# Performance work log

Hardware: AMD Instinct MI355X
Metric: run time of the kernel (lower is better)

## Reference

```python
import jax, jax.numpy as jnp
import numpy as np

N = 50000      # nodes
E = 800000     # edges (avg degree 16)
D = 64         # node_feature_dim
ED = 1         # edge_feature_dim
H = 128        # hidden_dim
G = 128        # graphs in batch
L = 3          # n_conv
EPS = 1e-5     # batchnorm eps


def setup_inputs() -> dict:
    key = jax.random.key(0)
    ks = jax.random.split(key, 20)
    w = lambda k, shp: (jax.random.normal(k, shp, dtype=jnp.float32)
                        / np.float32(np.sqrt(shp[-2] if len(shp) > 1 else 1.0)))
    return {
        "atom_z": jax.random.randint(ks[0], (N,), 0, 100),
        "edge_index": jax.random.randint(ks[1], (2, E), 0, N),
        "edge_attr": jax.random.normal(ks[2], (E, ED), dtype=jnp.float32),
        "batch": jnp.sort(jax.random.randint(ks[3], (N,), 0, G)),
        "emb": jax.random.normal(ks[4], (100, D), dtype=jnp.float32),
        "edge_W1": w(ks[5], (L, 2 * D + ED, H)), "edge_b1": jnp.zeros((L, H)),
        "edge_W2": w(ks[6], (L, H, H)),          "edge_b2": jnp.zeros((L, H)),
        "node_W1": w(ks[7], (L, D + H, H)),      "node_b1": jnp.zeros((L, H)),
        "node_W2": w(ks[8], (L, H, D)),          "node_b2": jnp.zeros((L, D)),
        "bn_gamma": jnp.ones((L, D)),            "bn_beta": jnp.zeros((L, D)),
        "out_W1": w(ks[9], (D, H)),  "out_b1": jnp.zeros((H,)),
        "out_W2": w(ks[10], (H, 1)), "out_b2": jnp.zeros((1,)),
    }


def reference(atom_z, edge_index, edge_attr, batch, emb,
              edge_W1, edge_b1, edge_W2, edge_b2,
              node_W1, node_b1, node_W2, node_b2,
              bn_gamma, bn_beta, out_W1, out_b1, out_W2, out_b2):
    sp = jax.nn.softplus
    src, dst = edge_index[0], edge_index[1]  # PyG source_to_target: x_j = x[src], x_i = x[dst]
    x = emb[atom_z]                          # [N, D]
    for l in range(L):
        # --- CGConv layer l ---
        z = jnp.concatenate([x[dst], x[src], edge_attr], axis=-1)        # [E, 2D+ED]
        m = sp(sp(z @ edge_W1[l] + edge_b1[l]) @ edge_W2[l] + edge_b2[l])  # [E, H]
        aggr = jax.ops.segment_sum(m, dst, num_segments=N)               # [N, H]
        h = jnp.concatenate([x, aggr], axis=-1)                          # [N, D+H]
        x = sp(h @ node_W1[l] + node_b1[l]) @ node_W2[l] + node_b2[l] + x
        # --- BatchNorm1d (training-mode batch stats) ---
        mu = jnp.mean(x, axis=0)
        var = jnp.mean(jnp.square(x - mu), axis=0)
        x = bn_gamma[l] * (x - mu) * jax.lax.rsqrt(var + EPS) + bn_beta[l]
    # --- global mean pool over graphs ---
    sums = jax.ops.segment_sum(x, batch, num_segments=G)                 # [G, D]
    cnts = jax.ops.segment_sum(jnp.ones((N, 1), x.dtype), batch, num_segments=G)
    pooled = sums / jnp.maximum(cnts, 1.0)
    # --- output MLP (dropout is identity at eval) ---
    out = sp(pooled @ out_W1 + out_b1) @ out_W2 + out_b2                 # [G, 1]
    return out
```

## Files before the change

kernel.cpp:

```cpp
#include <hip/hip_runtime.h>
#include <hip/hip_bf16.h>

#define N_NODES 50000
#define N_EDGES 800000
#define DIM 64
#define HID 128
#define NGRAPH 128
#define BN_EPS 1e-5f

typedef __attribute__((ext_vector_type(8))) short short8;
typedef __attribute__((ext_vector_type(4))) short short4v;
typedef __attribute__((ext_vector_type(4))) float f32x4;
typedef __attribute__((ext_vector_type(4))) int int4v;

__device__ __forceinline__ float sp_(float v) {
    return fmaxf(v, 0.f) + __logf(1.f + __expf(-fabsf(v)));
}
__device__ __forceinline__ short bfb(float f) {
    __hip_bfloat16 h = __float2bfloat16(f);
    return __builtin_bit_cast(short, h);
}
__device__ __forceinline__ float b2f(short s) {
    unsigned u = ((unsigned)(unsigned short)s) << 16;
    return __builtin_bit_cast(float, u);
}

__global__ void k_embed(const int* __restrict__ az, const float* __restrict__ emb,
                        float* __restrict__ x, __hip_bfloat16* __restrict__ xb) {
    int idx = blockIdx.x * 256 + threadIdx.x;
    if (idx >= N_NODES * DIM) return;
    int n = idx >> 6;
    int d = idx & 63;
    float v = emb[az[n] * DIM + d];
    x[idx] = v;
    xb[idx] = __float2bfloat16(v);
}

__global__ void k_wprep(const float* __restrict__ src, short* __restrict__ dst,
                        int total, int nshift, int srcStride) {
    int l = blockIdx.y;
    int idx = blockIdx.x * 256 + threadIdx.x;
    if (idx >= total) return;
    int K = total >> nshift;
    int k = idx >> nshift;
    int n = idx & ((1 << nshift) - 1);
    dst[(size_t)l * total + n * K + k] = bfb(src[(size_t)l * srcStride + idx]);
}

__global__ void k_hist(const int* __restrict__ edst, int* __restrict__ deg) {
    int e = blockIdx.x * 256 + threadIdx.x;
    if (e < N_EDGES) atomicAdd(&deg[edst[e]], 1);
}

__global__ void k_scan(const int* __restrict__ deg, int* __restrict__ cursor) {
    __shared__ int wsum[16];
    __shared__ int carry;
    const int t = threadIdx.x, lane = t & 63, w = t >> 6;
    if (t == 0) carry = 0;
    __syncthreads();
    for (int base = 0; base < N_NODES; base += 1024) {
        int i = base + t;
        int v = (i < N_NODES) ? deg[i] : 0;
        int s = v;
#pragma unroll
        for (int off = 1; off < 64; off <<= 1) {
            int u = __shfl_up(s, off);
            if (lane >= off) s += u;
        }
        if (lane == 63) wsum[w] = s;
        __syncthreads();
        if (w == 0) {
            int ws = (lane < 16) ? wsum[lane] : 0;
#pragma unroll
            for (int off = 1; off < 16; off <<= 1) {
                int u = __shfl_up(ws, off);
                if (lane >= off) ws += u;
            }
            if (lane < 16) wsum[lane] = ws;
        }
        __syncthreads();
        int woff = (w == 0) ? 0 : wsum[w - 1];
        int excl = carry + woff + s - v;
        if (i < N_NODES) cursor[i] = excl;
        __syncthreads();
        if (t == 1023) carry += wsum[15];
        __syncthreads();
    }
}

__global__ void k_scatter(const int* __restrict__ esrc, const int* __restrict__ edst,
                          const float* __restrict__ eattr, int* __restrict__ cursor,
                          int4v* __restrict__ sedge) {
    int e = blockIdx.x * 256 + threadIdx.x;
    if (e >= N_EDGES) return;
    int d = edst[e];
    int pos = atomicAdd(&cursor[d], 1);
    int4v rec = {esrc[e], d, __builtin_bit_cast(int, eattr[e]), 0};
    sedge[pos] = rec;
}

__global__ void k_gbounds(const int* __restrict__ batch, int* __restrict__ gstart) {
    int g = threadIdx.x;
    if (g > NGRAPH) return;
    int lo = 0, hi = N_NODES;
    while (lo < hi) {
        int mid = (lo + hi) >> 1;
        if (batch[mid] < g) lo = mid + 1; else hi = mid;
    }
    gstart[g] = lo;
}

__launch_bounds__(512, 2)
__global__ void k_ab(const __hip_bfloat16* __restrict__ xb,
                     const short* __restrict__ w1T, const float* __restrict__ b1,
                     short* __restrict__ xab) {
    __shared__ short xt[64 * 64];
    __shared__ short ot[64 * 256];
    const int t = threadIdx.x;
    const int wid = t >> 6, lane = t & 63, lrow = lane & 15, lk = lane >> 4;
    const int col = wid * 16 + lrow;
    const int n0 = blockIdx.x * 64;

    short8 wa[2], wb[2];
#pragma unroll
    for (int ks = 0; ks < 2; ks++) {
        wa[ks] = *(const short8*)((const char*)w1T + col * 256 + ks * 64 + lk * 16);
        wb[ks] = *(const short8*)((const char*)w1T + col * 256 + 128 + ks * 64 + lk * 16);
    }
    const float b1v = b1[col];

    {
        int r = t >> 3, q = t & 7;
        int node = n0 + r;
        int4v v = {0, 0, 0, 0};
        if (node < N_NODES) v = *(const int4v*)(xb + (size_t)node * DIM + q * 8);
        *(int4v*)((char*)xt + r * 128 + ((q * 16) ^ ((r & 7) << 4))) = v;
    }
    __syncthreads();

    f32x4 aa[4], ab[4];
#pragma unroll
    for (int mi = 0; mi < 4; mi++) { aa[mi] = (f32x4){0.f,0.f,0.f,0.f}; ab[mi] = (f32x4){0.f,0.f,0.f,0.f}; }
#pragma unroll
    for (int ks = 0; ks < 2; ks++) {
        int kb = ks * 64 + lk * 16;
        short8 av[4];
#pragma unroll
        for (int mi = 0; mi < 4; mi++) {
            int row = mi * 16 + lrow;
            av[mi] = *(const short8*)((const char*)xt + row * 128 + (kb ^ ((row & 7) << 4)));
        }
#pragma unroll
        for (int mi = 0; mi < 4; mi++) {
            aa[mi] = __builtin_amdgcn_mfma_f32_16x16x32_bf16(av[mi], wa[ks], aa[mi], 0, 0, 0);
            ab[mi] = __builtin_amdgcn_mfma_f32_16x16x32_bf16(av[mi], wb[ks], ab[mi], 0, 0, 0);
        }
    }
#pragma unroll
    for (int mi = 0; mi < 4; mi++) {
#pragma unroll
        for (int rr = 0; rr < 4; rr++) {
            int row = mi * 16 + lk * 4 + rr;
            int swz = (row & 7) << 4;
            *(short*)((char*)ot + row * 512 + ((col * 2) ^ swz)) = bfb(aa[mi][rr] + b1v);
            *(short*)((char*)ot + row * 512 + 256 + ((col * 2) ^ swz)) = bfb(ab[mi][rr]);
        }
    }
    __syncthreads();
#pragma unroll
    for (int it = 0; it < 4; it++) {
        int idx = it * 8192 + t * 16;
        int row = idx >> 9, off = idx & 511;
        int node = n0 + row;
        if (node < N_NODES) {
            int base = off & 256, lo = off & 255;
            int4v v = *(const int4v*)((char*)ot + row * 512 + base + (lo ^ ((row & 7) << 4)));
            *(int4v*)((char*)xab + (size_t)node * 512 + off) = v;
        }
    }
}

__launch_bounds__(512, 4)
__global__ void k_edge(const short* __restrict__ xab,
                       const int4v* __restrict__ sedge,
                       const float* __restrict__ wl, const float* __restrict__ b2,
                       const short* __restrict__ w2T,
                       float* __restrict__ aggr) {
    __shared__ short ht[64 * 128];
    __shared__ float mt[64 * 128];
    __shared__ int   dst_s[64];
    __shared__ int   seg_start[65];
    __shared__ int   seg_dst[64];
    __shared__ int   nseg_s;

    const int t = threadIdx.x;
    const int wid = t >> 6, lane = t & 63;
    const int lrow = lane & 15, lk = lane >> 4;
    const int r = t >> 3, q = t & 7;
    const int col = wid * 16 + lrow;

    short8 w2f[4];
#pragma unroll
    for (int ks = 0; ks < 4; ks++)
        w2f[ks] = *(const short8*)((const char*)w2T + col * 256 + ks * 64 + lk * 16);
    const float b2v = b2[col];
    float wlv[16];
#pragma unroll
    for (int i = 0; i < 16; i++) wlv[i] = wl[q * 16 + i];

    const int NT = N_EDGES / 64;
    const int tile0 = (int)(((long)blockIdx.x * NT) / 1000);
    const int tile1 = (int)(((long)(blockIdx.x + 1) * NT) / 1000);

    int4v ei;
    short8 ra0, ra1, rb0, rb1;
    {
        int e = tile0 * 64 + r;
        ei = sedge[e];
        const char* pa = (const char*)xab + (size_t)ei[1] * 512 + q * 32;
        const char* pb = (const char*)xab + (size_t)ei[0] * 512 + 256 + q * 32;
        ra0 = *(const short8*)pa;  ra1 = *(const short8*)(pa + 16);
        rb0 = *(const short8*)pb;  rb1 = *(const short8*)(pb + 16);
    }

    for (int tile = tile0; tile < tile1; ++tile) {
        {
            float at = __builtin_bit_cast(float, ei[2]);
            if (q == 0) dst_s[r] = ei[1];
            short8 h0, h1;
#pragma unroll
            for (int i = 0; i < 8; i++) {
                h0[i] = bfb(sp_(b2f(ra0[i]) + b2f(rb0[i]) + at * wlv[i]));
                h1[i] = bfb(sp_(b2f(ra1[i]) + b2f(rb1[i]) + at * wlv[8 + i]));
            }
            int swz = (r & 7) << 4;
            *(short8*)((char*)ht + r * 256 + ((q * 32) ^ swz)) = h0;
            *(short8*)((char*)ht + r * 256 + (((q * 32) + 16) ^ swz)) = h1;
        }
        __syncthreads();

        if (wid == 0) {
            int d = dst_s[lane];
            int prev = (lane == 0) ? -1 : dst_s[lane - 1];
            bool start = (d != prev);
            unsigned long long mask = __ballot(start);
            int sidx = __popcll(mask & ((1ull << lane) - 1));
            if (start) { seg_start[sidx] = lane; seg_dst[sidx] = d; }
            if (lane == 63) {
                int ns = __popcll(mask);
                nseg_s = ns;
                seg_start[ns] = 64;
            }
        }

        f32x4 acc2[4];
#pragma unroll
        for (int mi = 0; mi < 4; mi++) acc2[mi] = (f32x4){0.f, 0.f, 0.f, 0.f};
#pragma unroll
        for (int ks = 0; ks < 4; ks++) {
            int kb = ks * 64 + lk * 16;
            short8 av[4];
#pragma unroll
            for (int mi = 0; mi < 4; mi++) {
                int row = mi * 16 + lrow;
                av[mi] = *(const short8*)((const char*)ht + row * 256 + (kb ^ ((row & 7) << 4)));
            }
#pragma unroll
            for (int mi = 0; mi < 4; mi++)
                acc2[mi] = __builtin_amdgcn_mfma_f32_16x16x32_bf16(av[mi], w2f[ks], acc2[mi], 0, 0, 0);
        }
#pragma unroll
        for (int mi = 0; mi < 4; mi++) {
#pragma unroll
            for (int rr = 0; rr < 4; rr++) {
                int row = mi * 16 + lk * 4 + rr;
                *(float*)((char*)mt + row * 512 + ((col * 4) ^ ((row & 7) << 4))) = sp_(acc2[mi][rr] + b2v);
            }
        }
        __syncthreads();

        if (tile + 1 < tile1) {
            int e = (tile + 1) * 64 + r;
            ei = sedge[e];
            const char* pa = (const char*)xab + (size_t)ei[1] * 512 + q * 32;
            const char* pb = (const char*)xab + (size_t)ei[0] * 512 + 256 + q * 32;
            ra0 = *(const short8*)pa;  ra1 = *(const short8*)(pa + 16);
            rb0 = *(const short8*)pb;  rb1 = *(const short8*)(pb + 16);
        }

        {
            int nseg = nseg_s;
            int rcol = t & 127, h = t >> 7;
            for (int s = h; s < nseg; s += 4) {
                int r0 = seg_start[s], r1 = seg_start[s + 1];
                float sum = 0.f;
                for (int rr = r0; rr < r1; rr++)
                    sum += *(const float*)((const char*)mt + rr * 512 + ((rcol * 4) ^ ((rr & 7) << 4)));
                atomicAdd(&aggr[(size_t)seg_dst[s] * HID + rcol], sum);
            }
        }
    }
}

__launch_bounds__(256, 3)
__global__ void k_node(const __hip_bfloat16* __restrict__ xb,
                       const float* __restrict__ xf,
                       const float* __restrict__ aggr,
                       const short* __restrict__ w1T, const float* __restrict__ b1,
                       const short* __restrict__ w2T, const float* __restrict__ b2,
                       float* __restrict__ y, float* __restrict__ stats) {
    __shared__ short at[64 * 192];
    __shared__ short ht[64 * 128];

    const int t = threadIdx.x;
    const int wid = t >> 6, lane = t & 63, lrow = lane & 15, lk = lane >> 4;
    const int n0 = blockIdx.x * 64;

    const int nc0 = wid * 32;
    short8 w1f[6][2];
    float b1v[2];
#pragma unroll
    for (int ni = 0; ni < 2; ni++) {
        int col = nc0 + ni * 16 + lrow;
#pragma unroll
        for (int ks = 0; ks < 6; ks++) {
            int kb = ks * 64 + lk * 16;
            w1f[ks][ni] = *(const short8*)((const char*)w1T + col * 384 + kb);
        }
        b1v[ni] = b1[col];
    }
    const int nc2 = wid * 16;
    const int col2 = nc2 + lrow;
    short8 w2f[4];
#pragma unroll
    for (int ks = 0; ks < 4; ks++)
        w2f[ks] = *(const short8*)((const char*)w2T + col2 * 256 + ks * 64 + lk * 16);
    const float b2v = b2[col2];

    if (t < 64) {
        int node = n0 + t;
        if (node < N_NODES) {
            const __hip_bfloat16* xr = xb + (size_t)node * DIM;
#pragma unroll
            for (int i = 0; i < 8; i++) {
                int4v v = *(const int4v*)(xr + i * 8);
                *(int4v*)((char*)at + t * 384 + ((i * 16) ^ ((t & 7) << 4))) = v;
            }
        } else {
            int4v z = {0, 0, 0, 0};
#pragma unroll
            for (int i = 0; i < 8; i++)
                *(int4v*)((char*)at + t * 384 + ((i * 16) ^ ((t & 7) << 4))) = z;
        }
    }
    {
        int r = t >> 2, q = t & 3;
        int node = n0 + r;
#pragma unroll
        for (int i = 0; i < 4; i++) {
            short8 s = {0, 0, 0, 0, 0, 0, 0, 0};
            if (node < N_NODES) {
                const float* ar = aggr + (size_t)node * HID + q * 32 + i * 8;
                float4 f0 = *(const float4*)ar;
                float4 f1 = *(const float4*)(ar + 4);
                s = (short8){bfb(f0.x), bfb(f0.y), bfb(f0.z), bfb(f0.w),
                             bfb(f1.x), bfb(f1.y), bfb(f1.z), bfb(f1.w)};
            }
            int cb = 128 + q * 64 + i * 16;
            *(short8*)((char*)at + r * 384 + (cb ^ ((r & 7) << 4))) = s;
        }
    }
    __syncthreads();

    f32x4 acc[4][2];
#pragma unroll
    for (int mi = 0; mi < 4; mi++)
#pragma unroll
        for (int ni = 0; ni < 2; ni++) acc[mi][ni] = (f32x4){0.f, 0.f, 0.f, 0.f};
#pragma unroll
    for (int ks = 0; ks < 6; ks++) {
        int kb = ks * 64 + lk * 16;
        short8 av[4];
#pragma unroll
        for (int mi = 0; mi < 4; mi++) {
            int row = mi * 16 + lrow;
            av[mi] = *(const short8*)((const char*)at + row * 384 + (kb ^ ((row & 7) << 4)));
        }
#pragma unroll
        for (int mi = 0; mi < 4; mi++)
#pragma unroll
            for (int ni = 0; ni < 2; ni++)
                acc[mi][ni] = __builtin_amdgcn_mfma_f32_16x16x32_bf16(av[mi], w1f[ks][ni], acc[mi][ni], 0, 0, 0);
    }
#pragma unroll
    for (int mi = 0; mi < 4; mi++) {
#pragma unroll
        for (int ni = 0; ni < 2; ni++) {
            int col = nc0 + ni * 16 + lrow;
#pragma unroll
            for (int rr = 0; rr < 4; rr++) {
                int row = mi * 16 + lk * 4 + rr;
                float val = sp_(acc[mi][ni][rr] + b1v[ni]);
                *(short*)((char*)ht + row * 256 + ((col * 2) ^ ((row & 7) << 4))) = bfb(val);
            }
        }
    }
    __syncthreads();

    f32x4 acc2[4];
#pragma unroll
    for (int mi = 0; mi < 4; mi++) acc2[mi] = (f32x4){0.f, 0.f, 0.f, 0.f};
#pragma unroll
    for (int ks = 0; ks < 4; ks++) {
        int kb = ks * 64 + lk * 16;
        short8 av[4];
#pragma unroll
        for (int mi = 0; mi < 4; mi++) {
            int row = mi * 16 + lrow;
            av[mi] = *(const short8*)((const char*)ht + row * 256 + (kb ^ ((row & 7) << 4)));
        }
#pragma unroll
        for (int mi = 0; mi < 4; mi++)
            acc2[mi] = __builtin_amdgcn_mfma_f32_16x16x32_bf16(av[mi], w2f[ks], acc2[mi], 0, 0, 0);
    }
    float s1 = 0.f, s2 = 0.f;
#pragma unroll
    for (int mi = 0; mi < 4; mi++) {
#pragma unroll
        for (int rr = 0; rr < 4; rr++) {
            int row = mi * 16 + lk * 4 + rr;
            int node = n0 + row;
            if (node < N_NODES) {
                float v = acc2[mi][rr] + b2v + xf[(size_t)node * DIM + col2];
                y[(size_t)node * DIM + col2] = v;
                s1 += v;
                s2 += v * v;
            }
        }
    }
    s1 += __shfl_xor(s1, 16); s1 += __shfl_xor(s1, 32);
    s2 += __shfl_xor(s2, 16); s2 += __shfl_xor(s2, 32);
    if (lane < 16) {
        atomicAdd(&stats[col2], s1);
        atomicAdd(&stats[64 + col2], s2);
    }
}

__global__ void k_bnfin(const float* __restrict__ gamma, const float* __restrict__ beta,
                        float* __restrict__ stats) {
    int d = threadIdx.x;
    float mu = stats[d] * (1.f / N_NODES);
    float var = stats[64 + d] * (1.f / N_NODES) - mu * mu;
    float rstd = rsqrtf(var + BN_EPS);
    float a = gamma[d] * rstd;
    stats[128 + d] = a;
    stats[192 + d] = beta[d] - mu * a;
}

__global__ void k_bnapply(const float* __restrict__ y, const float* __restrict__ stats,
                          float* __restrict__ x, __hip_bfloat16* __restrict__ xb) {
    int idx = (blockIdx.x * 256 + threadIdx.x) * 4;
    if (idx >= N_NODES * DIM) return;
    int d = idx & 63;
    float4 v = *(const float4*)(y + idx);
    float4 r;
    r.x = stats[128 + d + 0] * v.x + stats[192 + d + 0];
    r.y = stats[128 + d + 1] * v.y + stats[192 + d + 1];
    r.z = stats[128 + d + 2] * v.z + stats[192 + d + 2];
    r.w = stats[128 + d + 3] * v.w + stats[192 + d + 3];
    *(float4*)(x + idx) = r;
    short4v s = {bfb(r.x), bfb(r.y), bfb(r.z), bfb(r.w)};
    *(short4v*)((char*)(xb + idx)) = s;
}

__global__ void k_pool2(const int* __restrict__ gstart, const float* __restrict__ x,
                        float* __restrict__ pooled) {
    __shared__ float red[256];
    const int g = blockIdx.x, t = threadIdx.x;
    const int d = t & 63, nl = t >> 6;
    const int s = gstart[g], e = gstart[g + 1];
    float sum = 0.f;
    for (int n = s + nl; n < e; n += 4)
        sum += x[(size_t)n * DIM + d];
    red[t] = sum;
    __syncthreads();
    if (t < 64) {
        float tot = red[t] + red[t + 64] + red[t + 128] + red[t + 192];
        int c = e - s;
        pooled[g * DIM + t] = tot / fmaxf((float)c, 1.f);
    }
}

__global__ void k_out(const float* __restrict__ pooled,
                      const float* __restrict__ W1, const float* __restrict__ b1,
                      const float* __restrict__ W2, const float* __restrict__ b2,
                      float* __restrict__ out) {
    __shared__ float pl[64];
    __shared__ float wsum[2];
    int g = blockIdx.x, t = threadIdx.x;
    if (t < 64) pl[t] = pooled[g * 64 + t];
    __syncthreads();
    float a = b1[t];
#pragma unroll
    for (int d = 0; d < 64; d++) a += pl[d] * W1[d * 128 + t];
    float c = sp_(a) * W2[t];
#pragma unroll
    for (int off = 32; off >= 1; off >>= 1) c += __shfl_down(c, off);
    int lane = t & 63, wid = t >> 6;
    if (lane == 0) wsum[wid] = c;
    __syncthreads();
    if (t == 0) out[g] = wsum[0] + wsum[1] + b2[0];
}

extern "C" void kernel_launch(void* const* d_in, const int* in_sizes, int n_in,
                              void* d_out, int out_size, void* d_ws, size_t ws_size,
                              hipStream_t stream) {
    const int*   az    = (const int*)d_in[0];
    const int*   ei    = (const int*)d_in[1];
    const float* eattr = (const float*)d_in[2];
    const int*   batch = (const int*)d_in[3];
    const float* emb   = (const float*)d_in[4];
    const float* eW1   = (const float*)d_in[5];
    const float* eb1   = (const float*)d_in[6];
    const float* eW2   = (const float*)d_in[7];
    const float* eb2   = (const float*)d_in[8];
    const float* nW1   = (const float*)d_in[9];
    const float* nb1   = (const float*)d_in[10];
    const float* nW2   = (const float*)d_in[11];
    const float* nb2   = (const float*)d_in[12];
    const float* gam   = (const float*)d_in[13];
    const float* bet   = (const float*)d_in[14];
    const float* oW1   = (const float*)d_in[15];
    const float* ob1   = (const float*)d_in[16];
    const float* oW2   = (const float*)d_in[17];
    const float* ob2   = (const float*)d_in[18];
    const int* esrc = ei;
    const int* edst = ei + N_EDGES;

    float* x     = (float*)d_ws;
    float* y     = x + (size_t)N_NODES * DIM;
    float* aggr  = y + (size_t)N_NODES * DIM;
    float* stats = aggr + (size_t)N_NODES * HID;
    float* pooled = stats + 256;
    __hip_bfloat16* xb = (__hip_bfloat16*)(pooled + NGRAPH * DIM);
    short* ew1T = (short*)(xb + (size_t)N_NODES * DIM);
    short* ew2T = ew1T + 3 * 128 * 128;
    short* nw1T = ew2T + 3 * 128 * 128;
    short* nw2T = nw1T + 3 * 128 * 192;
    int*   cursor = (int*)(nw2T + 3 * 64 * 128);
    int4v* sedge  = (int4v*)(cursor + N_NODES + 48);
    int*   gstart = (int*)(sedge + N_EDGES);
    short* xab    = (short*)(gstart + 256);

    k_embed<<<(N_NODES * DIM + 255) / 256, 256, 0, stream>>>(az, emb, x, xb);

    k_wprep<<<dim3(64, 3), 256, 0, stream>>>(eW1, ew1T, 128 * 128, 7, 129 * 128);
    k_wprep<<<dim3(64, 3), 256, 0, stream>>>(eW2, ew2T, 128 * 128, 7, 128 * 128);
    k_wprep<<<dim3(96, 3), 256, 0, stream>>>(nW1, nw1T, 192 * 128, 7, 192 * 128);
    k_wprep<<<dim3(32, 3), 256, 0, stream>>>(nW2, nw2T, 128 * 64, 6, 128 * 64);

    hipMemsetAsync(cursor, 0, N_NODES * sizeof(int), stream);
    k_hist<<<(N_EDGES + 255) / 256, 256, 0, stream>>>(edst, cursor);
    k_scan<<<1, 1024, 0, stream>>>(cursor, cursor);
    k_scatter<<<(N_EDGES + 255) / 256, 256, 0, stream>>>(esrc, edst, eattr, cursor, sedge);
    k_gbounds<<<1, 256, 0, stream>>>(batch, gstart);

    for (int l = 0; l < 3; l++) {
        hipMemsetAsync(aggr, 0, ((size_t)N_NODES * HID + 256) * sizeof(float), stream);
        k_ab<<<(N_NODES + 63) / 64, 512, 0, stream>>>(xb, ew1T + (size_t)l * 128 * 128,
                                                      eb1 + l * 128, xab);
        k_edge<<<1000, 512, 0, stream>>>(xab, sedge,
                                         eW1 + (size_t)l * 129 * 128 + 128 * 128,
                                         eb2 + l * 128,
                                         ew2T + (size_t)l * 128 * 128,
                                         aggr);
        k_node<<<(N_NODES + 63) / 64, 256, 0, stream>>>(xb, x, aggr,
                                                        nw1T + (size_t)l * 128 * 192, nb1 + l * 128,
                                                        nw2T + (size_t)l * 64 * 128, nb2 + l * 64,
                                                        y, stats);
        k_bnfin<<<1, 64, 0, stream>>>(gam + l * 64, bet + l * 64, stats);
        k_bnapply<<<(N_NODES * DIM / 4 + 255) / 256, 256, 0, stream>>>(y, stats, x, xb);
    }

    k_pool2<<<NGRAPH, 256, 0, stream>>>(gstart, x, pooled);
    k_out<<<NGRAPH, 128, 0, stream>>>(pooled, oW1, ob1, oW2, ob2, (float*)d_out);
}
```

Baseline: 956.7 us.

## Fuse BatchNorm finalize and apply into next layer's edge-projection and pooling kernels

Removes the separate k_bnfin and k_bnapply launches. Each layer after the first now starts with k_abF, which computes the BatchNorm affine from the accumulated stats, writes x and xb, and runs the edge-projection MFMA in one pass. The last layer's normalization is folded into global mean pooling, since the affine map commutes with the mean. This saves launches and a full read/write pass over the node features. Separately, k_edge's launch_bounds occupancy hint rises from 4 to 6 blocks, which tightens register limits and could cause spills.

```diff
diff --git a/kernel.cpp b/kernel.cpp
--- a/kernel.cpp
+++ b/kernel.cpp
@@ -180,7 +180,102 @@
     }
 }
 
-__launch_bounds__(512, 4)
+__launch_bounds__(512, 2)
+__global__ void k_abF(const float* __restrict__ y,
+                      const float* __restrict__ stats,
+                      const float* __restrict__ gamma, const float* __restrict__ beta,
+                      const short* __restrict__ w1T, const float* __restrict__ b1,
+                      float* __restrict__ x, __hip_bfloat16* __restrict__ xb,
+                      short* __restrict__ xab) {
+    __shared__ short xt[64 * 64];
+    __shared__ short ot[64 * 256];
+    const int t = threadIdx.x;
+    const int wid = t >> 6, lane = t & 63, lrow = lane & 15, lk = lane >> 4;
+    const int col = wid * 16 + lrow;
+    const int n0 = blockIdx.x * 64;
+
+    short8 wa[2], wb[2];
+#pragma unroll
+    for (int ks = 0; ks < 2; ks++) {
+        wa[ks] = *(const short8*)((const char*)w1T + col * 256 + ks * 64 + lk * 16);
+        wb[ks] = *(const short8*)((const char*)w1T + col * 256 + 128 + ks * 64 + lk * 16);
+    }
+    const float b1v = b1[col];
+
+    {
+        int r = t >> 3, q = t & 7;
+        int node = n0 + r;
+        short8 s = {0, 0, 0, 0, 0, 0, 0, 0};
+        if (node < N_NODES) {
+            const float* yr = y + (size_t)node * DIM + q * 8;
+            float4 f0 = *(const float4*)yr;
+            float4 f1 = *(const float4*)(yr + 4);
+            float v[8] = {f0.x, f0.y, f0.z, f0.w, f1.x, f1.y, f1.z, f1.w};
+            float o[8];
+#pragma unroll
+            for (int i = 0; i < 8; i++) {
+                int d = q * 8 + i;
+                float mu = stats[d] * (1.f / N_NODES);
+                float var = stats[64 + d] * (1.f / N_NODES) - mu * mu;
+                float rstd = rsqrtf(var + BN_EPS);
+                float a = gamma[d] * rstd;
+                float b = beta[d] - mu * a;
+                o[i] = a * v[i] + b;
+                s[i] = bfb(o[i]);
+            }
+            float4 g0 = {o[0], o[1], o[2], o[3]};
+            float4 g1 = {o[4], o[5], o[6], o[7]};
+            *(float4*)(x + (size_t)node * DIM + q * 8) = g0;
+            *(float4*)(x + (size_t)node * DIM + q * 8 + 4) = g1;
+            *(short8*)((char*)xb + ((size_t)node * DIM + q * 8) * 2) = s;
+        }
+        *(int4v*)((char*)xt + r * 128 + ((q * 16) ^ ((r & 7) << 4))) = __builtin_bit_cast(int4v, s);
+    }
+    __syncthreads();
+
+    f32x4 aa[4], ab[4];
+#pragma unroll
+    for (int mi = 0; mi < 4; mi++) { aa[mi] = (f32x4){0.f,0.f,0.f,0.f}; ab[mi] = (f32x4){0.f,0.f,0.f,0.f}; }
+#pragma unroll
+    for (int ks = 0; ks < 2; ks++) {
+        int kb = ks * 64 + lk * 16;
+        short8 av[4];
+#pragma unroll
+        for (int mi = 0; mi < 4; mi++) {
+            int row = mi * 16 + lrow;
+            av[mi] = *(const short8*)((const char*)xt + row * 128 + (kb ^ ((row & 7) << 4)));
+        }
+#pragma unroll
+        for (int mi = 0; mi < 4; mi++) {
+            aa[mi] = __builtin_amdgcn_mfma_f32_16x16x32_bf16(av[mi], wa[ks], aa[mi], 0, 0, 0);
+            ab[mi] = __builtin_amdgcn_mfma_f32_16x16x32_bf16(av[mi], wb[ks], ab[mi], 0, 0, 0);
+        }
+    }
+#pragma unroll
+    for (int mi = 0; mi < 4; mi++) {
+#pragma unroll
+        for (int rr = 0; rr < 4; rr++) {
+            int row = mi * 16 + lk * 4 + rr;
+            int swz = (row & 7) << 4;
+            *(short*)((char*)ot + row * 512 + ((col * 2) ^ swz)) = bfb(aa[mi][rr] + b1v);
+            *(short*)((char*)ot + row * 512 + 256 + ((col * 2) ^ swz)) = bfb(ab[mi][rr]);
+        }
+    }
+    __syncthreads();
+#pragma unroll
+    for (int it = 0; it < 4; it++) {
+        int idx = it * 8192 + t * 16;
+        int row = idx >> 9, off = idx & 511;
+        int node = n0 + row;
+        if (node < N_NODES) {
+            int base = off & 256, lo = off & 255;
+            int4v v = *(const int4v*)((char*)ot + row * 512 + base + (lo ^ ((row & 7) << 4)));
+            *(int4v*)((char*)xab + (size_t)node * 512 + off) = v;
+        }
+    }
+}
+
+__launch_bounds__(512, 6)
 __global__ void k_edge(const short* __restrict__ xab,
                        const int4v* __restrict__ sedge,
                        const float* __restrict__ wl, const float* __restrict__ b2,
@@ -446,34 +541,9 @@
     }
 }
 
-__global__ void k_bnfin(const float* __restrict__ gamma, const float* __restrict__ beta,
-                        float* __restrict__ stats) {
-    int d = threadIdx.x;
-    float mu = stats[d] * (1.f / N_NODES);
-    float var = stats[64 + d] * (1.f / N_NODES) - mu * mu;
-    float rstd = rsqrtf(var + BN_EPS);
-    float a = gamma[d] * rstd;
-    stats[128 + d] = a;
-    stats[192 + d] = beta[d] - mu * a;
-}
-
-__global__ void k_bnapply(const float* __restrict__ y, const float* __restrict__ stats,
-                          float* __restrict__ x, __hip_bfloat16* __restrict__ xb) {
-    int idx = (blockIdx.x * 256 + threadIdx.x) * 4;
-    if (idx >= N_NODES * DIM) return;
-    int d = idx & 63;
-    float4 v = *(const float4*)(y + idx);
-    float4 r;
-    r.x = stats[128 + d + 0] * v.x + stats[192 + d + 0];
-    r.y = stats[128 + d + 1] * v.y + stats[192 + d + 1];
-    r.z = stats[128 + d + 2] * v.z + stats[192 + d + 2];
-    r.w = stats[128 + d + 3] * v.w + stats[192 + d + 3];
-    *(float4*)(x + idx) = r;
-    short4v s = {bfb(r.x), bfb(r.y), bfb(r.z), bfb(r.w)};
-    *(short4v*)((char*)(xb + idx)) = s;
-}
-
-__global__ void k_pool2(const int* __restrict__ gstart, const float* __restrict__ x,
+__global__ void k_pool2(const int* __restrict__ gstart, const float* __restrict__ y,
+                        const float* __restrict__ stats,
+                        const float* __restrict__ gamma, const float* __restrict__ beta,
                         float* __restrict__ pooled) {
     __shared__ float red[256];
     const int g = blockIdx.x, t = threadIdx.x;
@@ -481,13 +551,19 @@
     const int s = gstart[g], e = gstart[g + 1];
     float sum = 0.f;
     for (int n = s + nl; n < e; n += 4)
-        sum += x[(size_t)n * DIM + d];
+        sum += y[(size_t)n * DIM + d];
     red[t] = sum;
     __syncthreads();
     if (t < 64) {
         float tot = red[t] + red[t + 64] + red[t + 128] + red[t + 192];
         int c = e - s;
-        pooled[g * DIM + t] = tot / fmaxf((float)c, 1.f);
+        float mean = tot / fmaxf((float)c, 1.f);
+        float mu = stats[t] * (1.f / N_NODES);
+        float var = stats[64 + t] * (1.f / N_NODES) - mu * mu;
+        float rstd = rsqrtf(var + BN_EPS);
+        float a = gamma[t] * rstd;
+        float b = beta[t] - mu * a;
+        pooled[g * DIM + t] = a * mean + b;
     }
 }
 
@@ -566,9 +642,14 @@
     k_gbounds<<<1, 256, 0, stream>>>(batch, gstart);
 
     for (int l = 0; l < 3; l++) {
+        if (l == 0)
+            k_ab<<<(N_NODES + 63) / 64, 512, 0, stream>>>(xb, ew1T, eb1, xab);
+        else
+            k_abF<<<(N_NODES + 63) / 64, 512, 0, stream>>>(y, stats,
+                                                           gam + (l - 1) * 64, bet + (l - 1) * 64,
+                                                           ew1T + (size_t)l * 128 * 128, eb1 + l * 128,
+                                                           x, xb, xab);
         hipMemsetAsync(aggr, 0, ((size_t)N_NODES * HID + 256) * sizeof(float), stream);
-        k_ab<<<(N_NODES + 63) / 64, 512, 0, stream>>>(xb, ew1T + (size_t)l * 128 * 128,
-                                                      eb1 + l * 128, xab);
         k_edge<<<1000, 512, 0, stream>>>(xab, sedge,
                                          eW1 + (size_t)l * 129 * 128 + 128 * 128,
                                          eb2 + l * 128,
@@ -578,10 +659,8 @@
                                                         nw1T + (size_t)l * 128 * 192, nb1 + l * 128,
                                                         nw2T + (size_t)l * 64 * 128, nb2 + l * 64,
                                                         y, stats);
-        k_bnfin<<<1, 64, 0, stream>>>(gam + l * 64, bet + l * 64, stats);
-        k_bnapply<<<(N_NODES * DIM / 4 + 255) / 256, 256, 0, stream>>>(y, stats, x, xb);
-    }
-
-    k_pool2<<<NGRAPH, 256, 0, stream>>>(gstart, x, pooled);
+    }
+
+    k_pool2<<<NGRAPH, 256, 0, stream>>>(gstart, y, stats, gam + 2 * 64, bet + 2 * 64, pooled);
     k_out<<<NGRAPH, 128, 0, stream>>>(pooled, oW1, ob1, oW2, ob2, (float*)d_out);
 }
```

After: 1.374 ms. 43.6% more time.
